# Optimization experiments

Measured on AMD Instinct MI355X. Metric: run time of the kernel, lower is better.

Reference implementation:

```python
import jax, jax.numpy as jnp
import numpy as np

PATCH_SIZES = [4, 8, 16]
B, S, D, H = 32, 1000, 64, 512


def setup_inputs() -> dict:
    key = jax.random.key(0)
    ks = jax.random.split(key, 8)
    inp = {"x": jax.random.normal(ks[0], (B, S, D), dtype=jnp.float32)}
    for i, p in enumerate(PATCH_SIZES):
        fan_in = p * D
        inp[f"W{i}"] = jax.random.normal(ks[1 + 2 * i], (H, fan_in), dtype=jnp.float32) / np.sqrt(fan_in).astype(np.float32)
        inp[f"b{i}"] = jax.random.normal(ks[2 + 2 * i], (H,), dtype=jnp.float32) * 0.01
    inp["pos"] = jax.random.normal(ks[7], (1, 1000, H), dtype=jnp.float32)
    return inp


def reference(x, W0, b0, W1, b1, W2, b2, pos):
    Ws = [W0, W1, W2]
    bs = [b0, b1, b2]
    batch, seq_len, d = x.shape
    min_len = seq_len - max(PATCH_SIZES) + 1  # all scales truncated to this
    embs = []
    for p, W, b in zip(PATCH_SIZES, Ws, bs):
        # sliding windows, stride 1, only the first min_len windows are kept
        idx = jnp.arange(min_len)[:, None] + jnp.arange(p)[None, :]  # (min_len, p)
        win = x[:, idx, :]  # (batch, min_len, p, d) -- im2col gather
        # torch Linear on flattened [time, feature] patch: W[h, t*d + f]
        Wk = W.reshape(-1, p, d)  # (H, p, d)
        embs.append(jnp.einsum('blpd,hpd->blh', win, Wk) + b)
    out = jnp.stack(embs, axis=1).mean(axis=1)  # mean over scales
    return out + pos[:, :min_len, :]
```

## Files before the change

### kernel.cpp

```cpp
#include <hip/hip_runtime.h>
#include <stdint.h>

typedef unsigned short u16;
typedef __attribute__((ext_vector_type(8))) short bf16x8;
typedef __attribute__((ext_vector_type(8))) u16  u16x8;
typedef __attribute__((ext_vector_type(4))) float f32x4;

static constexpr int BATCH  = 32;
static constexpr int SEQ    = 1000;
static constexpr int DIM    = 64;
static constexpr int HOUT   = 512;
static constexpr int MINLEN = 985;
static constexpr int AROWS  = 144;

static constexpr size_t PB_OFF = 0;
static constexpr size_t WF_OFF = 4u << 20;

__device__ inline u16 f2bf(float f) {
  union { float f; uint32_t u; } v; v.f = f;
  uint32_t r = v.u + 0x7fffu + ((v.u >> 16) & 1u);
  return (u16)(r >> 16);
}

__global__ void pe_prep(const float* __restrict__ W0, const float* __restrict__ W1,
                        const float* __restrict__ W2, const float* __restrict__ b0,
                        const float* __restrict__ b1, const float* __restrict__ b2,
                        const float* __restrict__ pos,
                        u16* __restrict__ Wp, float* __restrict__ posb) {
  int bid = blockIdx.x;
  if (bid < 256) {
    int j  = bid * 256 + threadIdx.x;
    int h  = j >> 7;
    int kc = j & 127;
    float v[8];
    const float4* w2 = (const float4*)(W2 + h * 1024 + kc * 8);
    float4 a = w2[0], c = w2[1];
    v[0]=a.x; v[1]=a.y; v[2]=a.z; v[3]=a.w; v[4]=c.x; v[5]=c.y; v[6]=c.z; v[7]=c.w;
    if (kc < 64) {
      const float4* w1 = (const float4*)(W1 + h * 512 + kc * 8);
      float4 d = w1[0], e = w1[1];
      v[0]+=d.x; v[1]+=d.y; v[2]+=d.z; v[3]+=d.w; v[4]+=e.x; v[5]+=e.y; v[6]+=e.z; v[7]+=e.w;
    }
    if (kc < 32) {
      const float4* w0 = (const float4*)(W0 + h * 256 + kc * 8);
      float4 d = w0[0], e = w0[1];
      v[0]+=d.x; v[1]+=d.y; v[2]+=d.z; v[3]+=d.w; v[4]+=e.x; v[5]+=e.y; v[6]+=e.z; v[7]+=e.w;
    }
    u16x8 o;
    #pragma unroll
    for (int e = 0; e < 8; ++e) o[e] = f2bf(v[e] * (1.0f / 3.0f));
    size_t dst = ((size_t)(h >> 4) * 32 + (kc >> 2)) * 512 + (kc & 3) * 128 + (h & 15) * 8;
    *(u16x8*)(Wp + dst) = o;
  } else {
    int idx = (bid - 256) * 256 + threadIdx.x;
    if (idx < MINLEN * (HOUT / 4)) {
      int l  = idx >> 7;
      int h4 = idx & 127;
      float4 p  = ((const float4*)pos)[(size_t)l * 128 + h4];
      float4 a0 = ((const float4*)b0)[h4];
      float4 a1 = ((const float4*)b1)[h4];
      float4 a2 = ((const float4*)b2)[h4];
      float4 o;
      o.x = p.x + (a0.x + a1.x + a2.x) * (1.0f / 3.0f);
      o.y = p.y + (a0.y + a1.y + a2.y) * (1.0f / 3.0f);
      o.z = p.z + (a0.z + a1.z + a2.z) * (1.0f / 3.0f);
      o.w = p.w + (a0.w + a1.w + a2.w) * (1.0f / 3.0f);
      ((float4*)posb)[idx] = o;
    }
  }
}

__global__ __launch_bounds__(256, 4) void pe_gemm(
    const float* __restrict__ x, const u16* __restrict__ Wp,
    const float* __restrict__ posb, float* __restrict__ out) {
  __shared__ u16 ldsA[AROWS * 64];

  const int t    = threadIdx.x;
  const int w    = t >> 6;
  const int lane = t & 63;

  const int sw = (blockIdx.x & 7) * 128 + (blockIdx.x >> 3);
  const int n0 = (sw & 3) * 128;
  const int l0 = ((sw >> 2) & 7) * 128;
  const int b  = sw >> 5;

  const int wr   = w >> 1;
  const int wc   = w & 1;
  const int lr   = lane & 15;
  const int g    = lane >> 4;

  const u16* Bp = Wp + ((size_t)((n0 >> 4) + wc * 4) * 32) * 512 + lane * 8;

  const float* Ax = x + (size_t)b * (SEQ * DIM) + (size_t)l0 * 64;
  #pragma unroll
  for (int it = 0; it < 5; ++it) {
    int idx = it * 256 + t;
    if (idx < AROWS * 8) {
      int row = idx >> 3, ch = idx & 7;
      u16x8 o;
      if (l0 + row < SEQ) {
        const float4* p = (const float4*)(Ax + row * 64 + ch * 8);
        float4 a = p[0], c = p[1];
        o[0] = f2bf(a.x); o[1] = f2bf(a.y); o[2] = f2bf(a.z); o[3] = f2bf(a.w);
        o[4] = f2bf(c.x); o[5] = f2bf(c.y); o[6] = f2bf(c.z); o[7] = f2bf(c.w);
      } else {
        o = (u16x8)(0);
      }
      *(u16x8*)&ldsA[row * 64 + (ch ^ (row & 7)) * 8] = o;
    }
  }

  bf16x8 bA[4], bB[4];
  #pragma unroll
  for (int n = 0; n < 4; ++n)
    bA[n] = *(const bf16x8*)(Bp + (size_t)(n * 32) * 512);

  __syncthreads();

  f32x4 acc[4][4] = {};
  const int rbase = wr * 64 + lr;

  #define A_READS(kt_, aF_)                                                   \
    _Pragma("unroll")                                                         \
    for (int m = 0; m < 4; ++m) {                                             \
      int r = rbase + m * 16 + ((kt_) >> 1);                                  \
      int s = ((((kt_) & 1) << 2) + g) ^ (r & 7);                             \
      aF_[m] = *(const bf16x8*)&ldsA[r * 64 + s * 8];                         \
    }
  #define B_LOADS(kt_, dst_)                                                  \
    _Pragma("unroll")                                                         \
    for (int n = 0; n < 4; ++n)                                               \
      dst_[n] = *(const bf16x8*)(Bp + (size_t)(n * 32 + (kt_)) * 512);
  #define MFMAS(aF_, bF_)                                                     \
    __builtin_amdgcn_s_setprio(1);                                            \
    _Pragma("unroll")                                                         \
    for (int m = 0; m < 4; ++m)                                               \
      _Pragma("unroll")                                                       \
      for (int n = 0; n < 4; ++n)                                             \
        acc[m][n] = __builtin_amdgcn_mfma_f32_16x16x32_bf16(aF_[m], bF_[n],   \
                                                            acc[m][n], 0, 0, 0); \
    __builtin_amdgcn_s_setprio(0);

  for (int kt = 0; kt < 32; kt += 2) {
    bf16x8 aF[8];
    if (kt + 1 < 32) { B_LOADS(kt + 1, bB); }
    A_READS(kt, aF);
    MFMAS(aF, bA);
    if (kt + 2 < 32) { B_LOADS(kt + 2, bA); }
    A_READS(kt + 1, aF);
    MFMAS(aF, bB);
  }
  #undef A_READS
  #undef B_LOADS
  #undef MFMAS

  #pragma unroll
  for (int n = 0; n < 4; ++n) {
    const int h = n0 + wc * 64 + n * 16 + lr;
    #pragma unroll
    for (int m = 0; m < 4; ++m) {
      const int rowb = l0 + wr * 64 + m * 16 + (g << 2);
      #pragma unroll
      for (int r = 0; r < 4; ++r) {
        const int l = rowb + r;
        if (l < MINLEN) {
          out[((size_t)b * MINLEN + l) * HOUT + h] =
              acc[m][n][r] + posb[(size_t)l * HOUT + h];
        }
      }
    }
  }
}

extern "C" void kernel_launch(void* const* d_in, const int* in_sizes, int n_in,
                              void* d_out, int out_size, void* d_ws, size_t ws_size,
                              hipStream_t stream) {
  const float* x   = (const float*)d_in[0];
  const float* W0  = (const float*)d_in[1];
  const float* b0  = (const float*)d_in[2];
  const float* W1  = (const float*)d_in[3];
  const float* b1  = (const float*)d_in[4];
  const float* W2  = (const float*)d_in[5];
  const float* b2  = (const float*)d_in[6];
  const float* pos = (const float*)d_in[7];
  float* out = (float*)d_out;

  char*  ws   = (char*)d_ws;
  float* posb = (float*)(ws + PB_OFF);
  u16*   Wp   = (u16*)(ws + WF_OFF);

  hipLaunchKernelGGL(pe_prep, dim3(256 + 493), dim3(256), 0, stream,
                     W0, W1, W2, b0, b1, b2, pos, Wp, posb);
  hipLaunchKernelGGL(pe_gemm, dim3(1024), dim3(256), 0, stream,
                     x, Wp, posb, out);
}
```

Measured before the change: 64.16 us.

## Pre-convert x to bf16 in prep kernel and read A fragments directly from global

The x to bf16 conversion moves out of the GEMM into the prep kernel, which writes a padded bf16 copy of x to workspace. The GEMM then drops its LDS staging and __syncthreads and loads A fragments straight from global/L2 memory. The launch also becomes a 3D grid, which removes the swizzled block mapping. This adds a full extra write and read of x in bf16 and relies on the cache to absorb the overlapping sliding-window row reads.

```diff
diff --git a/kernel.cpp b/kernel.cpp
--- a/kernel.cpp
+++ b/kernel.cpp
@@ -11,10 +11,11 @@
 static constexpr int DIM    = 64;
 static constexpr int HOUT   = 512;
 static constexpr int MINLEN = 985;
-static constexpr int AROWS  = 144;
 
 static constexpr size_t PB_OFF = 0;
-static constexpr size_t WF_OFF = 4u << 20;
+static constexpr size_t XB_OFF = 2u << 20;
+static constexpr size_t WF_OFF = 8u << 20;
+static constexpr int    XB_TOTAL = 2048000 + 8192;
 
 __device__ inline u16 f2bf(float f) {
   union { float f; uint32_t u; } v; v.f = f;
@@ -22,14 +23,28 @@
   return (u16)(r >> 16);
 }
 
-__global__ void pe_prep(const float* __restrict__ W0, const float* __restrict__ W1,
+__global__ void pe_prep(const float* __restrict__ x,
+                        const float* __restrict__ W0, const float* __restrict__ W1,
                         const float* __restrict__ W2, const float* __restrict__ b0,
                         const float* __restrict__ b1, const float* __restrict__ b2,
                         const float* __restrict__ pos,
-                        u16* __restrict__ Wp, float* __restrict__ posb) {
+                        u16* __restrict__ xb, u16* __restrict__ Wp,
+                        float* __restrict__ posb) {
   int bid = blockIdx.x;
-  if (bid < 256) {
-    int j  = bid * 256 + threadIdx.x;
+  if (bid < 1004) {
+    int i = (bid * 256 + threadIdx.x) * 8;
+    u16x8 o;
+    if (i < 2048000) {
+      const float4* p = (const float4*)(x + i);
+      float4 a = p[0], c = p[1];
+      o[0] = f2bf(a.x); o[1] = f2bf(a.y); o[2] = f2bf(a.z); o[3] = f2bf(a.w);
+      o[4] = f2bf(c.x); o[5] = f2bf(c.y); o[6] = f2bf(c.z); o[7] = f2bf(c.w);
+    } else {
+      o = (u16x8)(0);
+    }
+    *(u16x8*)(xb + i) = o;
+  } else if (bid < 1260) {
+    int j  = (bid - 1004) * 256 + threadIdx.x;
     int h  = j >> 7;
     int kc = j & 127;
     float v[8];
@@ -52,7 +67,7 @@
     size_t dst = ((size_t)(h >> 4) * 32 + (kc >> 2)) * 512 + (kc & 3) * 128 + (h & 15) * 8;
     *(u16x8*)(Wp + dst) = o;
   } else {
-    int idx = (bid - 256) * 256 + threadIdx.x;
+    int idx = (bid - 1260) * 256 + threadIdx.x;
     if (idx < MINLEN * (HOUT / 4)) {
       int l  = idx >> 7;
       int h4 = idx & 127;
@@ -71,62 +86,35 @@
 }
 
 __global__ __launch_bounds__(256, 4) void pe_gemm(
-    const float* __restrict__ x, const u16* __restrict__ Wp,
+    const u16* __restrict__ xb, const u16* __restrict__ Wp,
     const float* __restrict__ posb, float* __restrict__ out) {
-  __shared__ u16 ldsA[AROWS * 64];
-
   const int t    = threadIdx.x;
   const int w    = t >> 6;
   const int lane = t & 63;
-
-  const int sw = (blockIdx.x & 7) * 128 + (blockIdx.x >> 3);
-  const int n0 = (sw & 3) * 128;
-  const int l0 = ((sw >> 2) & 7) * 128;
-  const int b  = sw >> 5;
-
+  const int b    = blockIdx.z;
+  const int l0   = blockIdx.y * 128;
+  const int n0   = blockIdx.x * 128;
   const int wr   = w >> 1;
   const int wc   = w & 1;
   const int lr   = lane & 15;
   const int g    = lane >> 4;
 
   const u16* Bp = Wp + ((size_t)((n0 >> 4) + wc * 4) * 32) * 512 + lane * 8;
-
-  const float* Ax = x + (size_t)b * (SEQ * DIM) + (size_t)l0 * 64;
-  #pragma unroll
-  for (int it = 0; it < 5; ++it) {
-    int idx = it * 256 + t;
-    if (idx < AROWS * 8) {
-      int row = idx >> 3, ch = idx & 7;
-      u16x8 o;
-      if (l0 + row < SEQ) {
-        const float4* p = (const float4*)(Ax + row * 64 + ch * 8);
-        float4 a = p[0], c = p[1];
-        o[0] = f2bf(a.x); o[1] = f2bf(a.y); o[2] = f2bf(a.z); o[3] = f2bf(a.w);
-        o[4] = f2bf(c.x); o[5] = f2bf(c.y); o[6] = f2bf(c.z); o[7] = f2bf(c.w);
-      } else {
-        o = (u16x8)(0);
-      }
-      *(u16x8*)&ldsA[row * 64 + (ch ^ (row & 7)) * 8] = o;
-    }
-  }
+  const u16* Ap = xb + (size_t)b * (SEQ * DIM)
+                     + (size_t)(l0 + wr * 64 + lr) * 64 + g * 8;
 
   bf16x8 bA[4], bB[4];
   #pragma unroll
   for (int n = 0; n < 4; ++n)
     bA[n] = *(const bf16x8*)(Bp + (size_t)(n * 32) * 512);
 
-  __syncthreads();
-
   f32x4 acc[4][4] = {};
-  const int rbase = wr * 64 + lr;
 
   #define A_READS(kt_, aF_)                                                   \
     _Pragma("unroll")                                                         \
-    for (int m = 0; m < 4; ++m) {                                             \
-      int r = rbase + m * 16 + ((kt_) >> 1);                                  \
-      int s = ((((kt_) & 1) << 2) + g) ^ (r & 7);                             \
-      aF_[m] = *(const bf16x8*)&ldsA[r * 64 + s * 8];                         \
-    }
+    for (int m = 0; m < 4; ++m)                                               \
+      aF_[m] = *(const bf16x8*)(Ap + (m * 16 + ((kt_) >> 1)) * 64             \
+                                   + ((kt_) & 1) * 32);
   #define B_LOADS(kt_, dst_)                                                  \
     _Pragma("unroll")                                                         \
     for (int n = 0; n < 4; ++n)                                               \
@@ -142,7 +130,7 @@
     __builtin_amdgcn_s_setprio(0);
 
   for (int kt = 0; kt < 32; kt += 2) {
-    bf16x8 aF[8];
+    bf16x8 aF[4];
     if (kt + 1 < 32) { B_LOADS(kt + 1, bB); }
     A_READS(kt, aF);
     MFMAS(aF, bA);
@@ -187,10 +175,11 @@
 
   char*  ws   = (char*)d_ws;
   float* posb = (float*)(ws + PB_OFF);
+  u16*   xbf  = (u16*)(ws + XB_OFF);
   u16*   Wp   = (u16*)(ws + WF_OFF);
 
-  hipLaunchKernelGGL(pe_prep, dim3(256 + 493), dim3(256), 0, stream,
-                     W0, W1, W2, b0, b1, b2, pos, Wp, posb);
-  hipLaunchKernelGGL(pe_gemm, dim3(1024), dim3(256), 0, stream,
-                     x, Wp, posb, out);
+  hipLaunchKernelGGL(pe_prep, dim3(1004 + 256 + 493), dim3(256), 0, stream,
+                     x, W0, W1, W2, b0, b1, b2, pos, xbf, Wp, posb);
+  hipLaunchKernelGGL(pe_gemm, dim3(HOUT / 128, 8, BATCH), dim3(256), 0, stream,
+                     xbf, Wp, posb, out);
 }
```

Measured after the change: 101.0 us. 1.57x slower.
